# Performance work log

Hardware: AMD Instinct MI355X
Metric: run time of the kernel (lower is better)

## Reference

```python
import jax, jax.numpy as jnp
import numpy as np

HEADS = 8

def setup_inputs() -> dict:
    key = jax.random.key(0)
    ks = jax.random.split(key, 5)
    B, S, C = 2, 4096, 640
    s = 1.0 / np.sqrt(C)
    return {
        "hidden_states": jax.random.normal(ks[0], (B, S, C), dtype=jnp.float32),
        "Wq": jax.random.normal(ks[1], (C, C), dtype=jnp.float32) * s,
        "bq": jnp.zeros((C,), dtype=jnp.float32),
        "Wk": jax.random.normal(ks[2], (C, C), dtype=jnp.float32) * s,
        "bk": jnp.zeros((C,), dtype=jnp.float32),
        "Wv": jax.random.normal(ks[3], (C, C), dtype=jnp.float32) * s,
        "bv": jnp.zeros((C,), dtype=jnp.float32),
        "Wo": jax.random.normal(ks[4], (C, C), dtype=jnp.float32) * s,
        "bo": jnp.zeros((C,), dtype=jnp.float32),
    }


def reference(hidden_states, Wq, bq, Wk, bk, Wv, bv, Wo, bo):
    # Self-attention (encoder_hidden_states=None), no mask, no norms.
    B, S, C = hidden_states.shape
    H = HEADS
    D = C // H  # head_dim
    residual = hidden_states

    q = hidden_states @ Wq + bq  # [B,S,C]
    k = hidden_states @ Wk + bk
    v = hidden_states @ Wv + bv

    # [B,S,C] -> [B,H,S,D]
    q = q.reshape(B, S, H, D).transpose(0, 2, 1, 3)
    k = k.reshape(B, S, H, D).transpose(0, 2, 1, 3)
    v = v.reshape(B, S, H, D).transpose(0, 2, 1, 3)

    scale = 1.0 / np.sqrt(D)
    scores = jnp.einsum('bhqd,bhkd->bhqk', q, k) * scale  # [B,H,S,S]
    probs = jax.nn.softmax(scores, axis=-1)               # materialized, as in source
    out = jnp.einsum('bhqk,bhkd->bhqd', probs, v)         # [B,H,S,D]

    out = out.transpose(0, 2, 1, 3).reshape(B, S, C)
    out = out @ Wo + bo  # to_out[0]; to_out[1] is dropout (identity in eval)
    out = out + residual  # residual_connection=True
    return out            # rescale_output_factor = 1.0
```

## Files before the change

### kernel.cpp

```cpp
#include <hip/hip_runtime.h>
#include <hip/hip_bf16.h>
#include <stdint.h>

typedef __attribute__((ext_vector_type(8))) short short8;
typedef __attribute__((ext_vector_type(4))) short short4v;
typedef __attribute__((ext_vector_type(4))) float f32x4;
typedef __attribute__((ext_vector_type(16))) float f32x16;
typedef unsigned short u16;
typedef unsigned int u32;

#define DEV __device__ __forceinline__

constexpr int Bb = 2, Ss = 4096, Cc = 640, Hh = 8, Dd = 80;
constexpr int BS = Bb * Ss;
constexpr int NQKV = 3 * Cc;
constexpr int QKst = 2 * Cc;

DEV float bf2f(u16 u) { unsigned v = ((unsigned)u) << 16; float f; __builtin_memcpy(&f, &v, 4); return f; }
DEV u16 f2bf(float f) {
    unsigned u; __builtin_memcpy(&u, &f, 4);
    u += 0x7fffu + ((u >> 16) & 1u);
    return (u16)(u >> 16);
}
DEV u32 packbf2(float a, float b) {
    float2 f2; f2.x = a; f2.y = b;
    __hip_bfloat162 h2 = __float22bfloat162_rn(f2);
    u32 r; __builtin_memcpy(&r, &h2, 4);
    return r;
}

DEV void pswapf(float &a, float &b) {
#if __has_builtin(__builtin_amdgcn_permlane32_swap)
    auto r = __builtin_amdgcn_permlane32_swap(__float_as_int(a), __float_as_int(b), false, false);
    a = __int_as_float(r[0]); b = __int_as_float(r[1]);
#else
    float sa = __shfl_xor(a, 32, 64), sb = __shfl_xor(b, 32, 64);
    bool hi = (threadIdx.x & 32) != 0;
    float na = hi ? sb : a, nb = hi ? b : sa;
    a = na; b = nb;
#endif
}

#define GLD16(gp, lp) __builtin_amdgcn_global_load_lds( \
    (const __attribute__((address_space(1))) void*)(gp), \
    (__attribute__((address_space(3))) void*)(lp), 16, 0, 0)

__global__ __launch_bounds__(256) void prep_kernel(
    const float* __restrict__ hs,
    const float* __restrict__ Wq, const float* __restrict__ Wk,
    const float* __restrict__ Wv, const float* __restrict__ Wo,
    const float* __restrict__ bq, const float* __restrict__ bk,
    const float* __restrict__ bv,
    u16* __restrict__ Xb, float* __restrict__ bcat,
    u16* __restrict__ WTqkv, u16* __restrict__ WTo)
{
    const float QS = 0.11180339887498949f * 1.4426950408889634f;
    if (blockIdx.x < 1600) {
        __shared__ float T[32][33];
        int tile = blockIdx.x;
        int wsel = tile / 400;
        int tt = tile - wsel * 400;
        int tr = tt / 20, tc = tt - (tt / 20) * 20;
        const float* W = (wsel == 0) ? Wq : (wsel == 1) ? Wk : (wsel == 2) ? Wv : Wo;
        float sc = (wsel == 0) ? QS : 1.0f;
        int r = threadIdx.x >> 3, c4 = (threadIdx.x & 7) * 4;
        float4 v = *(const float4*)(W + (size_t)(tr * 32 + r) * Cc + tc * 32 + c4);
        T[r][c4 + 0] = v.x; T[r][c4 + 1] = v.y; T[r][c4 + 2] = v.z; T[r][c4 + 3] = v.w;
        __syncthreads();
        short4v o;
#pragma unroll
        for (int j = 0; j < 4; j++) o[j] = (short)f2bf(T[c4 + j][r] * sc);
        u16* dst = (wsel < 3) ? (WTqkv + (size_t)(wsel * Cc + tc * 32 + r) * Cc + tr * 32 + c4)
                              : (WTo + (size_t)(tc * 32 + r) * Cc + tr * 32 + c4);
        *(short4v*)dst = o;
    } else {
        int tid = (blockIdx.x - 1600) * blockDim.x + threadIdx.x;
        int nthr = 2048 * blockDim.x;
        for (int i = tid; i < BS * Cc / 4; i += nthr) {
            float4 v = ((const float4*)hs)[i];
            short4v o;
            o[0] = (short)f2bf(v.x); o[1] = (short)f2bf(v.y);
            o[2] = (short)f2bf(v.z); o[3] = (short)f2bf(v.w);
            ((short4v*)Xb)[i] = o;
        }
        for (int i = tid; i < NQKV; i += nthr) {
            float v = (i < Cc) ? bq[i] * QS : (i < 2 * Cc) ? bk[i - Cc] : bv[i - 2 * Cc];
            bcat[i] = v;
        }
    }
}

__global__ __launch_bounds__(256) void gemm_qkv(
    const u16* __restrict__ A, const u16* __restrict__ Bt,
    const float* __restrict__ bias, u16* __restrict__ QK,
    u16* __restrict__ VTg)
{
    __shared__ __align__(16) char gsm[32768];

    const int mBase = blockIdx.x * 128;
    const int nBase = blockIdx.y * 128;
    const int t = threadIdx.x, lane = t & 63, w = t >> 6;
    const int wr = w >> 1, wc = w & 1;
    const int l15 = lane & 15, g = lane >> 4;

    const int r0 = t >> 2, r1 = (t + 256) >> 2;
    const int cg0 = (t & 3) ^ (r0 & 3);
    const int cg1 = (t & 3) ^ (r1 & 3);
    const u16* pa0 = A + (size_t)(mBase + r0) * Cc + cg0 * 8;
    const u16* pa1 = A + (size_t)(mBase + r1) * Cc + cg1 * 8;
    const u16* pb0 = Bt + (size_t)(nBase + r0) * Cc + cg0 * 8;
    const u16* pb1 = Bt + (size_t)(nBase + r1) * Cc + cg1 * 8;

    auto stage = [&](int k0, int buf) {
        GLD16(pa0 + k0, gsm + buf * 8192 + w * 1024);
        GLD16(pa1 + k0, gsm + buf * 8192 + 4096 + w * 1024);
        GLD16(pb0 + k0, gsm + 16384 + buf * 8192 + w * 1024);
        GLD16(pb1 + k0, gsm + 16384 + buf * 8192 + 4096 + w * 1024);
    };

    stage(0, 0);
    __syncthreads();

    f32x4 acc[4][4] = {};
    const int lof = l15 * 64 + ((g ^ (l15 & 3)) << 4);
    int cur = 0;

    for (int k0 = 0; k0 < Cc; k0 += 32) {
        if (k0 + 32 < Cc) stage(k0 + 32, cur ^ 1);
        short8 af[4], bf[4];
#pragma unroll
        for (int i = 0; i < 4; i++) {
            af[i] = *(const short8*)(gsm + cur * 8192 + wr * 4096 + i * 1024 + lof);
            bf[i] = *(const short8*)(gsm + 16384 + cur * 8192 + wc * 4096 + i * 1024 + lof);
        }
#pragma unroll
        for (int mi = 0; mi < 4; mi++)
#pragma unroll
            for (int ni = 0; ni < 4; ni++)
                acc[mi][ni] = __builtin_amdgcn_mfma_f32_16x16x32_bf16(af[mi], bf[ni], acc[mi][ni], 0, 0, 0);
        __syncthreads();
        cur ^= 1;
    }

    if (nBase < 2 * Cc) {
#pragma unroll
        for (int mi = 0; mi < 4; mi++)
#pragma unroll
            for (int ni = 0; ni < 4; ni++) {
                int col = nBase + wc * 64 + ni * 16 + l15;
                float bb = bias[col];
#pragma unroll
                for (int r = 0; r < 4; r++) {
                    int row = mBase + wr * 64 + mi * 16 + g * 4 + r;
                    QK[(size_t)row * QKst + col] = f2bf(acc[mi][ni][r] + bb);
                }
            }
    } else {
        const int gp = ((g & 1) << 1) | (g >> 1);
#pragma unroll
        for (int mi = 0; mi < 4; mi++)
#pragma unroll
            for (int ni = 0; ni < 4; ni++) {
                int colg = nBase + wc * 64 + ni * 16 + l15;
                float bb = bias[colg];
                int vc = colg - 2 * Cc;
                int h = vc / Dd, d = vc - h * Dd;
                int row0 = mBase + wr * 64 + mi * 16 + gp * 4;
                int b = (mBase >> 12), s = row0 & 4095;
                short4v o;
#pragma unroll
                for (int r = 0; r < 4; r++) o[r] = (short)f2bf(acc[mi][ni][r] + bb);
                *(short4v*)(VTg + ((size_t)(b * Hh + h) * Dd + d) * Ss + s) = o;
            }
    }
}

constexpr int OBP = 88;

__global__ __launch_bounds__(256, 4) void attn_kernel(
    const u16* __restrict__ QK, const u16* __restrict__ VTg,
    u16* __restrict__ N0, u16* __restrict__ N1,
    float* __restrict__ Mp, float* __restrict__ Lp)
{
    __shared__ __align__(16) char smem[34816];

    const int id = blockIdx.x;
    const int qt = id >> 5;
    const int bh = (id & 31) >> 1;
    const int kvs = id & 1;
    const int b = bh >> 3, h = bh & 7;
    const int t = threadIdx.x, lane = t & 63, w = t >> 6;
    const int l31 = lane & 31, e = lane >> 5;

    const size_t rowBase = (size_t)b * Ss;
    const int q0 = qt * 128;
    const int kvBase = kvs * (Ss / 2);
    constexpr int NT = (Ss / 2) / 64;

    const int lq8 = lane >> 3;
    const int vcg = (lane & 7) ^ lq8;
    const u16* kg0 = QK + (rowBase + kvBase + lane) * QKst + Cc + h * Dd;
    const u16* vg0 = VTg + ((size_t)bh * Dd) * Ss + kvBase + vcg * 8;

    for (int i = t; i < 512; i += 256) {
        ((u32*)(smem + 10240 + 80 * 128))[i] = 0x3F803F80u;
        ((u32*)(smem + 10240 + 12288 + 80 * 128))[i] = 0x3F803F80u;
    }

    short8 qB[5];
    {
        const u16* qp = QK + (rowBase + q0 + w * 32 + l31) * QKst + h * Dd + e * 8;
#pragma unroll
        for (int ks = 0; ks < 5; ks++) qB[ks] = *(const short8*)(qp + ks * 16);
    }

    auto stageK = [&](int kt) {
#pragma unroll
        for (int j = 0; j < 3; j++) {
            int gi = w + 4 * j;
            if (gi < 10)
                GLD16(kg0 + (size_t)kt * 64 * QKst + gi * 8, smem + gi * 1024);
        }
    };
    auto stageV = [&](int kt, int vb) {
#pragma unroll
        for (int j = 0; j < 3; j++) {
            int gi = w + 4 * j;
            if (gi < 10)
                GLD16(vg0 + (size_t)(gi * 8 + lq8) * Ss + kt * 64,
                      smem + 10240 + vb * 12288 + gi * 1024);
        }
    };

    stageK(0);
    stageV(0, 0);
    __syncthreads();

    float mrow = -1e30f;
    f32x16 oacc[3] = {};
    int vcur = 0;
    const int csl_base = l31 & 7;

    for (int kt = 0; kt < NT; ++kt) {
        const bool more = (kt + 1 < NT);

        f32x16 s2[2];
        __builtin_amdgcn_s_setprio(1);
#pragma unroll
        for (int n = 0; n < 2; n++) {
            f32x16 a = {};
#pragma unroll
            for (int ks = 0; ks < 5; ks++) {
                short8 kf = *(const short8*)(smem + ((2 * ks + e) * 64 + n * 32 + l31) * 16);
                a = __builtin_amdgcn_mfma_f32_32x32x16_bf16(kf, qB[ks], a, 0, 0, 0);
            }
            s2[n] = a;
        }
        __builtin_amdgcn_s_setprio(0);

        __syncthreads();
        if (more) {
            stageK(kt + 1);
            stageV(kt + 1, vcur ^ 1);
        }

#define SV(j) ((j) < 16 ? s2[0][(j)] : s2[1][(j) - 16])
        float tt[11];
#pragma unroll
        for (int i = 0; i < 10; i++)
            tt[i] = fmaxf(fmaxf(SV(3 * i), SV(3 * i + 1)), SV(3 * i + 2));
        tt[10] = fmaxf(SV(30), SV(31));
#undef SV
        float u0 = fmaxf(fmaxf(tt[0], tt[1]), tt[2]);
        float u1 = fmaxf(fmaxf(tt[3], tt[4]), tt[5]);
        float u2 = fmaxf(fmaxf(tt[6], tt[7]), tt[8]);
        float u3 = fmaxf(tt[9], tt[10]);
        float vm = fmaxf(fmaxf(u0, u1), fmaxf(u2, u3));
        { float va = vm, vb = vm; pswapf(va, vb); vm = fmaxf(va, vb); }

        if (__any(vm > mrow + 8.0f)) {
            float mnew = fmaxf(mrow, vm);
            float al = __builtin_amdgcn_exp2f(mrow - mnew);
            mrow = mnew;
#pragma unroll
            for (int n = 0; n < 3; n++)
#pragma unroll
                for (int r = 0; r < 16; r++) oacc[n][r] *= al;
        }

        u32 pd[2][8];
#pragma unroll
        for (int n = 0; n < 2; n++)
#pragma unroll
            for (int m = 0; m < 8; m++) {
                float pa = __builtin_amdgcn_exp2f(s2[n][2 * m] - mrow);
                float pb = __builtin_amdgcn_exp2f(s2[n][2 * m + 1] - mrow);
                pd[n][m] = packbf2(pa, pb);
            }

        const char* vbase = smem + 10240 + vcur * 12288;
        __builtin_amdgcn_s_setprio(1);
#pragma unroll
        for (int ks = 0; ks < 4; ks++) {
            const int n = ks >> 1, bb2 = ks & 1;
            union { u32 u[4]; short8 v; } pB;
            pB.u[0] = pd[n][4 * bb2 + 0];
            pB.u[1] = pd[n][4 * bb2 + 1];
            pB.u[2] = pd[n][4 * bb2 + 2];
            pB.u[3] = pd[n][4 * bb2 + 3];
            const int csl = (2 * ks + e) ^ csl_base;
#pragma unroll
            for (int n2 = 0; n2 < 3; n2++) {
                short8 vf = *(const short8*)(vbase + ((n2 * 32 + l31) * 8 + csl) * 16);
                oacc[n2] = __builtin_amdgcn_mfma_f32_32x32x16_bf16(vf, pB.v, oacc[n2], 0, 0, 0);
            }
        }
        __builtin_amdgcn_s_setprio(0);

        __syncthreads();
        vcur ^= 1;
    }

    if (e == 0) {
        int mi = kvs * 65536 + bh * Ss + q0 + w * 32 + l31;
        Mp[mi] = mrow;
        Lp[mi] = oacc[2][8];
    }

    u16* Ob = (u16*)smem;
#pragma unroll
    for (int n = 0; n < 3; n++)
#pragma unroll
        for (int r = 0; r < 16; r += 2) {
            if (n == 2 && r >= 8) continue;
            int dloc = n * 32 + (r & 3) + 8 * (r >> 2) + 4 * e;
            u32 pk = packbf2(oacc[n][r], oacc[n][r + 1]);
            *(u32*)&Ob[(w * 32 + l31) * OBP + dloc] = pk;
        }
    __syncthreads();

    u16* Np = kvs ? N1 : N0;
    const int cb = h * Dd;
#pragma unroll
    for (int i = 0; i < 5; i++) {
        int gidx = i * 256 + t;
        int row = gidx / 10, gi = gidx % 10;
        short8 v = *(const short8*)&Ob[row * OBP + gi * 8];
        *(short8*)(Np + (rowBase + q0 + row) * Cc + cb + gi * 8) = v;
    }
}

__global__ __launch_bounds__(256) void gemm_oproj(
    const u16* __restrict__ N0, const u16* __restrict__ N1,
    const u16* __restrict__ Bt,
    const float* __restrict__ Mp, const float* __restrict__ Lp,
    const float* __restrict__ bias, const float* __restrict__ resid,
    float* __restrict__ Out)
{
    __shared__ __align__(16) char osm[28672];
    float* WF = (float*)(osm + 24576);

    const int mBase = blockIdx.x * 64;
    const int nBase = blockIdx.y * 128;
    const int t = threadIdx.x, lane = t & 63, w = t >> 6;
    const int wr = w >> 1, wc = w & 1;
    const int l15 = lane & 15, g = lane >> 4;

    for (int i = t; i < 512; i += 256) {
        int r = i >> 3, h = i & 7;
        int row = mBase + r;
        int bb = row >> 12, q = row & 4095;
        int mi = (bb * 8 + h) * Ss + q;
        float m0 = Mp[mi], m1 = Mp[65536 + mi];
        float l0 = Lp[mi], l1 = Lp[65536 + mi];
        float m = fmaxf(m0, m1);
        float w0 = exp2f(m0 - m), w1 = exp2f(m1 - m);
        float rl = 1.0f / (l0 * w0 + l1 * w1);
        WF[(r * 8 + h) * 2 + 0] = w0 * rl;
        WF[(r * 8 + h) * 2 + 1] = w1 * rl;
    }

    const int rA = t >> 2, clA = t & 3;
    const int cgA = clA ^ (rA & 3);
    const int rB0 = t >> 2, rB1 = (t + 256) >> 2;
    const int cgB0 = (t & 3) ^ (rB0 & 3);
    const int cgB1 = (t & 3) ^ (rB1 & 3);
    const u16* pA0 = N0 + (size_t)(mBase + rA) * Cc + cgA * 8;
    const u16* pA1 = N1 + (size_t)(mBase + rA) * Cc + cgA * 8;
    const u16* pB0 = Bt + (size_t)(nBase + rB0) * Cc + cgB0 * 8;
    const u16* pB1 = Bt + (size_t)(nBase + rB1) * Cc + cgB1 * 8;

    auto stageB = [&](int k0, int buf) {
        GLD16(pB0 + k0, osm + 8192 + buf * 8192 + w * 1024);
        GLD16(pB1 + k0, osm + 8192 + buf * 8192 + 4096 + w * 1024);
    };
    auto stageA = [&](int k0, int buf) {
        int kA = k0 + cgA * 8;
        int hA = kA / 80;
        float w0 = WF[(rA * 8 + hA) * 2], w1 = WF[(rA * 8 + hA) * 2 + 1];
        short8 a0 = *(const short8*)(pA0 + k0);
        short8 c0 = *(const short8*)(pA1 + k0);
        union { u32 u[4]; short8 v; } mg;
#pragma unroll
        for (int j = 0; j < 4; j++)
            mg.u[j] = packbf2(bf2f((u16)a0[2 * j]) * w0 + bf2f((u16)c0[2 * j]) * w1,
                              bf2f((u16)a0[2 * j + 1]) * w0 + bf2f((u16)c0[2 * j + 1]) * w1);
        *(short8*)(osm + buf * 4096 + rA * 64 + clA * 16) = mg.v;
    };

    __syncthreads();
    stageB(0, 0);
    stageA(0, 0);
    __syncthreads();

    f32x4 acc[2][4] = {};
    const int lof = l15 * 64 + ((g ^ (l15 & 3)) << 4);
    int cur = 0;

    for (int k0 = 0; k0 < Cc; k0 += 32) {
        const bool more = (k0 + 32 < Cc);
        if (more) stageB(k0 + 32, cur ^ 1);
        short8 af[2], bf[4];
#pragma unroll
        for (int i = 0; i < 2; i++)
            af[i] = *(const short8*)(osm + cur * 4096 + wr * 2048 + i * 1024 + lof);
#pragma unroll
        for (int i = 0; i < 4; i++)
            bf[i] = *(const short8*)(osm + 8192 + cur * 8192 + wc * 4096 + i * 1024 + lof);
#pragma unroll
        for (int mi = 0; mi < 2; mi++)
#pragma unroll
            for (int ni = 0; ni < 4; ni++)
                acc[mi][ni] = __builtin_amdgcn_mfma_f32_16x16x32_bf16(af[mi], bf[ni], acc[mi][ni], 0, 0, 0);
        if (more) stageA(k0 + 32, cur ^ 1);
        __syncthreads();
        cur ^= 1;
    }

#pragma unroll
    for (int mi = 0; mi < 2; mi++)
#pragma unroll
        for (int ni = 0; ni < 4; ni++) {
            int col = nBase + wc * 64 + ni * 16 + l15;
            float bb = bias[col];
#pragma unroll
            for (int r = 0; r < 4; r++) {
                int row = mBase + wr * 32 + mi * 16 + g * 4 + r;
                Out[(size_t)row * Cc + col] = acc[mi][ni][r] + bb + resid[(size_t)row * Cc + col];
            }
        }
}

extern "C" void kernel_launch(void* const* d_in, const int* in_sizes, int n_in,
                              void* d_out, int out_size, void* d_ws, size_t ws_size,
                              hipStream_t stream) {
    (void)in_sizes; (void)n_in; (void)out_size; (void)ws_size;
    const float* hs = (const float*)d_in[0];
    const float* Wq = (const float*)d_in[1];
    const float* bq = (const float*)d_in[2];
    const float* Wk = (const float*)d_in[3];
    const float* bk = (const float*)d_in[4];
    const float* Wv = (const float*)d_in[5];
    const float* bv = (const float*)d_in[6];
    const float* Wo = (const float*)d_in[7];
    const float* bo = (const float*)d_in[8];
    float* out = (float*)d_out;

    char* ws = (char*)d_ws;
    u16*   Xb    = (u16*)  (ws + 0);
    u16*   WTqkv = (u16*)  (ws + 10485760);
    u16*   WTo   = (u16*)  (ws + 12943360);
    float* bcat  = (float*)(ws + 13762560);
    u16*   QK    = (u16*)  (ws + 13770240);
    u16*   VTg   = (u16*)  (ws + 34741760);
    u16*   AOb   = (u16*)  (ws + 45227520);
    float* Mp    = (float*)(ws + 55713280);
    float* Lp    = (float*)(ws + 56237568);
    u16*   N1    = Xb;

    prep_kernel<<<dim3(3648), dim3(256), 0, stream>>>(hs, Wq, Wk, Wv, Wo, bq, bk, bv,
                                                      Xb, bcat, WTqkv, WTo);
    gemm_qkv<<<dim3(64, 15), dim3(256), 0, stream>>>(Xb, WTqkv, bcat, QK, VTg);
    attn_kernel<<<dim3(1024), dim3(256), 0, stream>>>(QK, VTg, AOb, N1, Mp, Lp);
    gemm_oproj<<<dim3(128, 5), dim3(256), 0, stream>>>(AOb, N1, WTo, Mp, Lp, bo, hs, out);
}
```

Baseline: 184.3 us.

## Split attention KV range three ways and single-buffer V to cut LDS

Attention work is now split across three KV segments instead of two when workspace allows, which raises the grid from 1024 to 1536 blocks. The o-proj merge combines three partial results with their max and sum statistics. V staging drops double-buffering to shrink LDS and raise occupancy, but V loads for the next tile are now issued only after the PV MMAs finish, so they overlap less with compute. The extra partial buffer adds more memory traffic in the merge step.

```diff
diff --git a/kernel.cpp b/kernel.cpp
--- a/kernel.cpp
+++ b/kernel.cpp
@@ -179,33 +179,34 @@
 
 __global__ __launch_bounds__(256, 4) void attn_kernel(
     const u16* __restrict__ QK, const u16* __restrict__ VTg,
-    u16* __restrict__ N0, u16* __restrict__ N1,
-    float* __restrict__ Mp, float* __restrict__ Lp)
+    u16* __restrict__ N0, u16* __restrict__ N1, u16* __restrict__ N2,
+    float* __restrict__ Mp, float* __restrict__ Lp, int ns)
 {
-    __shared__ __align__(16) char smem[34816];
+    __shared__ __align__(16) char smem[22528];
 
     const int id = blockIdx.x;
-    const int qt = id >> 5;
-    const int bh = (id & 31) >> 1;
-    const int kvs = id & 1;
+    const int per_qt = 16 * ns;
+    const int qt = id / per_qt;
+    const int rest = id - qt * per_qt;
+    const int bh = rest / ns;
+    const int si = rest - bh * ns;
     const int b = bh >> 3, h = bh & 7;
     const int t = threadIdx.x, lane = t & 63, w = t >> 6;
     const int l31 = lane & 31, e = lane >> 5;
 
     const size_t rowBase = (size_t)b * Ss;
     const int q0 = qt * 128;
-    const int kvBase = kvs * (Ss / 2);
-    constexpr int NT = (Ss / 2) / 64;
+    const int startT = (ns == 2) ? si * 32 : (si == 0 ? 0 : (si == 1 ? 22 : 43));
+    const int NT = (ns == 2) ? 32 : (si == 0 ? 22 : 21);
+    const int kvBase = startT * 64;
 
     const int lq8 = lane >> 3;
     const int vcg = (lane & 7) ^ lq8;
     const u16* kg0 = QK + (rowBase + kvBase + lane) * QKst + Cc + h * Dd;
     const u16* vg0 = VTg + ((size_t)bh * Dd) * Ss + kvBase + vcg * 8;
 
-    for (int i = t; i < 512; i += 256) {
-        ((u32*)(smem + 10240 + 80 * 128))[i] = 0x3F803F80u;
-        ((u32*)(smem + 10240 + 12288 + 80 * 128))[i] = 0x3F803F80u;
-    }
+    for (int i = t; i < 512; i += 256)
+        ((u32*)(smem + 20480))[i] = 0x3F803F80u;
 
     short8 qB[5];
     {
@@ -222,23 +223,22 @@
                 GLD16(kg0 + (size_t)kt * 64 * QKst + gi * 8, smem + gi * 1024);
         }
     };
-    auto stageV = [&](int kt, int vb) {
+    auto stageV = [&](int kt) {
 #pragma unroll
         for (int j = 0; j < 3; j++) {
             int gi = w + 4 * j;
             if (gi < 10)
                 GLD16(vg0 + (size_t)(gi * 8 + lq8) * Ss + kt * 64,
-                      smem + 10240 + vb * 12288 + gi * 1024);
+                      smem + 10240 + gi * 1024);
         }
     };
 
     stageK(0);
-    stageV(0, 0);
+    stageV(0);
     __syncthreads();
 
     float mrow = -1e30f;
     f32x16 oacc[3] = {};
-    int vcur = 0;
     const int csl_base = l31 & 7;
 
     for (int kt = 0; kt < NT; ++kt) {
@@ -259,10 +259,7 @@
         __builtin_amdgcn_s_setprio(0);
 
         __syncthreads();
-        if (more) {
-            stageK(kt + 1);
-            stageV(kt + 1, vcur ^ 1);
-        }
+        if (more) stageK(kt + 1);
 
 #define SV(j) ((j) < 16 ? s2[0][(j)] : s2[1][(j) - 16])
         float tt[11];
@@ -298,7 +295,6 @@
                 pd[n][m] = packbf2(pa, pb);
             }
 
-        const char* vbase = smem + 10240 + vcur * 12288;
         __builtin_amdgcn_s_setprio(1);
 #pragma unroll
         for (int ks = 0; ks < 4; ks++) {
@@ -311,18 +307,18 @@
             const int csl = (2 * ks + e) ^ csl_base;
 #pragma unroll
             for (int n2 = 0; n2 < 3; n2++) {
-                short8 vf = *(const short8*)(vbase + ((n2 * 32 + l31) * 8 + csl) * 16);
+                short8 vf = *(const short8*)(smem + 10240 + ((n2 * 32 + l31) * 8 + csl) * 16);
                 oacc[n2] = __builtin_amdgcn_mfma_f32_32x32x16_bf16(vf, pB.v, oacc[n2], 0, 0, 0);
             }
         }
         __builtin_amdgcn_s_setprio(0);
 
         __syncthreads();
-        vcur ^= 1;
+        if (more) stageV(kt + 1);
     }
 
     if (e == 0) {
-        int mi = kvs * 65536 + bh * Ss + q0 + w * 32 + l31;
+        int mi = si * 65536 + bh * Ss + q0 + w * 32 + l31;
         Mp[mi] = mrow;
         Lp[mi] = oacc[2][8];
     }
@@ -339,7 +335,7 @@
         }
     __syncthreads();
 
-    u16* Np = kvs ? N1 : N0;
+    u16* Np = (si == 0) ? N0 : ((si == 1) ? N1 : N2);
     const int cb = h * Dd;
 #pragma unroll
     for (int i = 0; i < 5; i++) {
@@ -352,12 +348,12 @@
 
 __global__ __launch_bounds__(256) void gemm_oproj(
     const u16* __restrict__ N0, const u16* __restrict__ N1,
-    const u16* __restrict__ Bt,
+    const u16* __restrict__ N2, const u16* __restrict__ Bt,
     const float* __restrict__ Mp, const float* __restrict__ Lp,
     const float* __restrict__ bias, const float* __restrict__ resid,
-    float* __restrict__ Out)
+    float* __restrict__ Out, int ns)
 {
-    __shared__ __align__(16) char osm[28672];
+    __shared__ __align__(16) char osm[30720];
     float* WF = (float*)(osm + 24576);
 
     const int mBase = blockIdx.x * 64;
@@ -372,12 +368,15 @@
         int bb = row >> 12, q = row & 4095;
         int mi = (bb * 8 + h) * Ss + q;
         float m0 = Mp[mi], m1 = Mp[65536 + mi];
+        float m2 = (ns == 3) ? Mp[131072 + mi] : -1e30f;
         float l0 = Lp[mi], l1 = Lp[65536 + mi];
-        float m = fmaxf(m0, m1);
-        float w0 = exp2f(m0 - m), w1 = exp2f(m1 - m);
-        float rl = 1.0f / (l0 * w0 + l1 * w1);
-        WF[(r * 8 + h) * 2 + 0] = w0 * rl;
-        WF[(r * 8 + h) * 2 + 1] = w1 * rl;
+        float l2 = (ns == 3) ? Lp[131072 + mi] : 1.0f;
+        float m = fmaxf(fmaxf(m0, m1), m2);
+        float w0 = exp2f(m0 - m), w1 = exp2f(m1 - m), w2 = exp2f(m2 - m);
+        float rl = 1.0f / (l0 * w0 + l1 * w1 + l2 * w2);
+        WF[(r * 8 + h) * 3 + 0] = w0 * rl;
+        WF[(r * 8 + h) * 3 + 1] = w1 * rl;
+        WF[(r * 8 + h) * 3 + 2] = w2 * rl;
     }
 
     const int rA = t >> 2, clA = t & 3;
@@ -387,6 +386,7 @@
     const int cgB1 = (t & 3) ^ (rB1 & 3);
     const u16* pA0 = N0 + (size_t)(mBase + rA) * Cc + cgA * 8;
     const u16* pA1 = N1 + (size_t)(mBase + rA) * Cc + cgA * 8;
+    const u16* pA2 = N2 + (size_t)(mBase + rA) * Cc + cgA * 8;
     const u16* pB0 = Bt + (size_t)(nBase + rB0) * Cc + cgB0 * 8;
     const u16* pB1 = Bt + (size_t)(nBase + rB1) * Cc + cgB1 * 8;
 
@@ -397,14 +397,17 @@
     auto stageA = [&](int k0, int buf) {
         int kA = k0 + cgA * 8;
         int hA = kA / 80;
-        float w0 = WF[(rA * 8 + hA) * 2], w1 = WF[(rA * 8 + hA) * 2 + 1];
+        float w0 = WF[(rA * 8 + hA) * 3], w1 = WF[(rA * 8 + hA) * 3 + 1],
+              w2 = WF[(rA * 8 + hA) * 3 + 2];
         short8 a0 = *(const short8*)(pA0 + k0);
         short8 c0 = *(const short8*)(pA1 + k0);
+        short8 d0 = *(const short8*)(pA2 + k0);
         union { u32 u[4]; short8 v; } mg;
 #pragma unroll
         for (int j = 0; j < 4; j++)
-            mg.u[j] = packbf2(bf2f((u16)a0[2 * j]) * w0 + bf2f((u16)c0[2 * j]) * w1,
-                              bf2f((u16)a0[2 * j + 1]) * w0 + bf2f((u16)c0[2 * j + 1]) * w1);
+            mg.u[j] = packbf2(
+                bf2f((u16)a0[2 * j]) * w0 + bf2f((u16)c0[2 * j]) * w1 + bf2f((u16)d0[2 * j]) * w2,
+                bf2f((u16)a0[2 * j + 1]) * w0 + bf2f((u16)c0[2 * j + 1]) * w1 + bf2f((u16)d0[2 * j + 1]) * w2);
         *(short8*)(osm + buf * 4096 + rA * 64 + clA * 16) = mg.v;
     };
 
@@ -454,7 +457,7 @@
 extern "C" void kernel_launch(void* const* d_in, const int* in_sizes, int n_in,
                               void* d_out, int out_size, void* d_ws, size_t ws_size,
                               hipStream_t stream) {
-    (void)in_sizes; (void)n_in; (void)out_size; (void)ws_size;
+    (void)in_sizes; (void)n_in; (void)out_size;
     const float* hs = (const float*)d_in[0];
     const float* Wq = (const float*)d_in[1];
     const float* bq = (const float*)d_in[2];
@@ -475,12 +478,16 @@
     u16*   VTg   = (u16*)  (ws + 34741760);
     u16*   AOb   = (u16*)  (ws + 45227520);
     float* Mp    = (float*)(ws + 55713280);
-    float* Lp    = (float*)(ws + 56237568);
+    float* Lp    = (float*)(ws + 56499712);
+    u16*   N2b   = (u16*)  (ws + 57286144);
     u16*   N1    = Xb;
+
+    const int ns = (ws_size >= 67771904ULL) ? 3 : 2;
+    u16* N2 = (ns == 3) ? N2b : AOb;
 
     prep_kernel<<<dim3(3648), dim3(256), 0, stream>>>(hs, Wq, Wk, Wv, Wo, bq, bk, bv,
                                                       Xb, bcat, WTqkv, WTo);
     gemm_qkv<<<dim3(64, 15), dim3(256), 0, stream>>>(Xb, WTqkv, bcat, QK, VTg);
-    attn_kernel<<<dim3(1024), dim3(256), 0, stream>>>(QK, VTg, AOb, N1, Mp, Lp);
-    gemm_oproj<<<dim3(128, 5), dim3(256), 0, stream>>>(AOb, N1, WTo, Mp, Lp, bo, hs, out);
-}
+    attn_kernel<<<dim3(32 * 16 * ns), dim3(256), 0, stream>>>(QK, VTg, AOb, N1, N2, Mp, Lp, ns);
+    gemm_oproj<<<dim3(128, 5), dim3(256), 0, stream>>>(AOb, N1, N2, WTo, Mp, Lp, bo, hs, out, ns);
+}
```

Result: no change. 185.2 us (+0.5%).

## Double-buffer K and V tiles with two-ahead prefetch in attention loop

Applied to the files above, without the earlier changes.

The attention kernel now keeps two full K+V tile buffers in LDS. Tiles kt and kt+1 are staged up front, and tile kt+2 is loaded after the single end-of-iteration barrier. This removes the mid-iteration __syncthreads and gives global loads a full iteration of lead time. In exchange, LDS per block grows and launch bounds drop to 3 blocks per CU, which lowers occupancy but may give the compiler more registers.

```diff
diff --git a/kernel.cpp b/kernel.cpp
--- a/kernel.cpp
+++ b/kernel.cpp
@@ -177,12 +177,12 @@
 
 constexpr int OBP = 88;
 
-__global__ __launch_bounds__(256, 4) void attn_kernel(
+__global__ __launch_bounds__(256, 3) void attn_kernel(
     const u16* __restrict__ QK, const u16* __restrict__ VTg,
     u16* __restrict__ N0, u16* __restrict__ N1,
     float* __restrict__ Mp, float* __restrict__ Lp)
 {
-    __shared__ __align__(16) char smem[34816];
+    __shared__ __align__(16) char smem[45056];
 
     const int id = blockIdx.x;
     const int qt = id >> 5;
@@ -204,7 +204,7 @@
 
     for (int i = t; i < 512; i += 256) {
         ((u32*)(smem + 10240 + 80 * 128))[i] = 0x3F803F80u;
-        ((u32*)(smem + 10240 + 12288 + 80 * 128))[i] = 0x3F803F80u;
+        ((u32*)(smem + 22528 + 10240 + 80 * 128))[i] = 0x3F803F80u;
     }
 
     short8 qB[5];
@@ -214,35 +214,38 @@
         for (int ks = 0; ks < 5; ks++) qB[ks] = *(const short8*)(qp + ks * 16);
     }
 
-    auto stageK = [&](int kt) {
+    auto stageK = [&](int kt, int buf) {
 #pragma unroll
         for (int j = 0; j < 3; j++) {
             int gi = w + 4 * j;
             if (gi < 10)
-                GLD16(kg0 + (size_t)kt * 64 * QKst + gi * 8, smem + gi * 1024);
+                GLD16(kg0 + (size_t)kt * 64 * QKst + gi * 8,
+                      smem + buf * 22528 + gi * 1024);
         }
     };
-    auto stageV = [&](int kt, int vb) {
+    auto stageV = [&](int kt, int buf) {
 #pragma unroll
         for (int j = 0; j < 3; j++) {
             int gi = w + 4 * j;
             if (gi < 10)
                 GLD16(vg0 + (size_t)(gi * 8 + lq8) * Ss + kt * 64,
-                      smem + 10240 + vb * 12288 + gi * 1024);
+                      smem + buf * 22528 + 10240 + gi * 1024);
         }
     };
 
-    stageK(0);
+    stageK(0, 0);
     stageV(0, 0);
+    stageK(1, 1);
+    stageV(1, 1);
     __syncthreads();
 
     float mrow = -1e30f;
     f32x16 oacc[3] = {};
-    int vcur = 0;
     const int csl_base = l31 & 7;
 
     for (int kt = 0; kt < NT; ++kt) {
-        const bool more = (kt + 1 < NT);
+        const char* kb = smem + (kt & 1) * 22528;
+        const char* vb = kb + 10240;
 
         f32x16 s2[2];
         __builtin_amdgcn_s_setprio(1);
@@ -251,18 +254,12 @@
             f32x16 a = {};
 #pragma unroll
             for (int ks = 0; ks < 5; ks++) {
-                short8 kf = *(const short8*)(smem + ((2 * ks + e) * 64 + n * 32 + l31) * 16);
+                short8 kf = *(const short8*)(kb + ((2 * ks + e) * 64 + n * 32 + l31) * 16);
                 a = __builtin_amdgcn_mfma_f32_32x32x16_bf16(kf, qB[ks], a, 0, 0, 0);
             }
             s2[n] = a;
         }
         __builtin_amdgcn_s_setprio(0);
-
-        __syncthreads();
-        if (more) {
-            stageK(kt + 1);
-            stageV(kt + 1, vcur ^ 1);
-        }
 
 #define SV(j) ((j) < 16 ? s2[0][(j)] : s2[1][(j) - 16])
         float tt[11];
@@ -276,7 +273,7 @@
         float u2 = fmaxf(fmaxf(tt[6], tt[7]), tt[8]);
         float u3 = fmaxf(tt[9], tt[10]);
         float vm = fmaxf(fmaxf(u0, u1), fmaxf(u2, u3));
-        { float va = vm, vb = vm; pswapf(va, vb); vm = fmaxf(va, vb); }
+        { float va = vm, vb2 = vm; pswapf(va, vb2); vm = fmaxf(va, vb2); }
 
         if (__any(vm > mrow + 8.0f)) {
             float mnew = fmaxf(mrow, vm);
@@ -298,7 +295,6 @@
                 pd[n][m] = packbf2(pa, pb);
             }
 
-        const char* vbase = smem + 10240 + vcur * 12288;
         __builtin_amdgcn_s_setprio(1);
 #pragma unroll
         for (int ks = 0; ks < 4; ks++) {
@@ -311,14 +307,17 @@
             const int csl = (2 * ks + e) ^ csl_base;
 #pragma unroll
             for (int n2 = 0; n2 < 3; n2++) {
-                short8 vf = *(const short8*)(vbase + ((n2 * 32 + l31) * 8 + csl) * 16);
+                short8 vf = *(const short8*)(vb + ((n2 * 32 + l31) * 8 + csl) * 16);
                 oacc[n2] = __builtin_amdgcn_mfma_f32_32x32x16_bf16(vf, pB.v, oacc[n2], 0, 0, 0);
             }
         }
         __builtin_amdgcn_s_setprio(0);
 
         __syncthreads();
-        vcur ^= 1;
+        if (kt + 2 < NT) {
+            stageK(kt + 2, kt & 1);
+            stageV(kt + 2, kt & 1);
+        }
     }
 
     if (e == 0) {
```

Result: faster. 177.8 us, median of 4 (-3.5%).
